# Optimization experiments

Measured on AMD Instinct MI355X. Metric: run time of the kernel, lower is better.

Reference implementation:

```python
import jax, jax.numpy as jnp
from jax import lax
import numpy as np

H, W = 28, 28
N = H * W
NMAX = 100

# gudhi CubicalComplex(top_dimensional_cells=f): lower-dim cells get the MIN of
# incident pixels (V-construction). Hence H0 of the sublevel filtration is
# connected components of pixels under 8-connectivity, where two components merge
# at the max of the connecting pixel values. H1 is computed by Alexander duality:
# dim-1 pairs of f  <->  finite dim-0 pairs of g=-f under 4-connectivity with a
# virtual outer node (g=-inf) attached to all boundary pixels; a g-pair (gb, gd)
# maps to an H1 pair (b, d) = (-gd, -gb).

def _pad_idx(Hh, Ww):
    idx = np.arange(Hh * Ww).reshape(Hh, Ww)
    p = np.full((Hh + 2, Ww + 2), -1, np.int64)
    p[1:-1, 1:-1] = idx
    return p

def _nbrs8(Hh, Ww):
    p = _pad_idx(Hh, Ww)
    dirs = [(-1, -1), (-1, 0), (-1, 1), (0, -1), (0, 1), (1, -1), (1, 0), (1, 1)]
    nb = np.full((Hh * Ww, 8), -1, np.int32)
    for k, (di, dj) in enumerate(dirs):
        nb[:, k] = p[1 + di:1 + di + Hh, 1 + dj:1 + dj + Ww].ravel()
    return nb

def _nbrs4v(Hh, Ww):
    # 4-connectivity + one slot pointing to the virtual outer node (index Hh*Ww)
    p = _pad_idx(Hh, Ww)
    dirs = [(-1, 0), (1, 0), (0, -1), (0, 1)]
    nb = np.full((Hh * Ww + 1, 5), -1, np.int32)
    for k, (di, dj) in enumerate(dirs):
        nb[:Hh * Ww, k] = p[1 + di:1 + di + Hh, 1 + dj:1 + dj + Ww].ravel()
    m = np.zeros((Hh, Ww), bool)
    m[0, :] = m[-1, :] = m[:, 0] = m[:, -1] = True
    nb[:Hh * Ww, 4] = np.where(m.ravel(), Hh * Ww, -1)
    return nb

NBRS8 = jnp.asarray(_nbrs8(H, W))
NBRS4V = jnp.asarray(_nbrs4v(H, W))

def _h0_deaths(values, nbrs):
    """Union-find over cells sorted by value; returns finite (birth, death) pairs
    (zero rows = unused slots). values: [M], nbrs: [M, K] int32 (-1 = none)."""
    M = values.shape[0]
    K = nbrs.shape[1]
    order = jnp.argsort(values)  # stable; rank = processing order (elder rule)
    rank = jnp.zeros(M, jnp.int32).at[order].set(jnp.arange(M, dtype=jnp.int32))

    def find(parent, i):
        def cond(s):
            return s[1][s[0]] != s[0]
        def body(s):
            i, p = s
            p = p.at[i].set(p[p[i]])  # path halving
            return (p[i], p)
        i, parent = lax.while_loop(cond, body, (i, parent))
        return parent, i

    def step(parent, r):
        c = order[r]
        deaths = jnp.zeros((K, 2), values.dtype)
        for k in range(K):  # fixed small unroll over neighbor slots
            n = nbrs[c, k]
            n_safe = jnp.maximum(n, 0)
            valid = (n >= 0) & (rank[n_safe] < r)  # only already-active neighbors
            parent, rc = find(parent, c)
            parent, rn = find(parent, jnp.where(valid, n_safe, c))
            merge = valid & (rc != rn)
            younger = jnp.where(rank[rc] > rank[rn], rc, rn)
            elder = jnp.where(rank[rc] > rank[rn], rn, rc)
            parent = parent.at[younger].set(jnp.where(merge, elder, younger))
            pair = jnp.stack([values[younger], values[c]])  # (birth, death)
            deaths = deaths.at[k].set(jnp.where(merge, pair, jnp.zeros(2, values.dtype)))
        return parent, deaths

    parent0 = jnp.arange(M, dtype=jnp.int32)
    _, deaths = lax.scan(step, parent0, jnp.arange(M, dtype=jnp.int32))
    return deaths.reshape(M * K, 2)

def _select_diag(pairs, nmax):
    # gudhi returns pairs sorted by decreasing persistence; min_persistence=0 drops
    # zero-persistence pairs. Pad with zeros to nmax (as the numpy diagram buffer).
    b, d = pairs[:, 0], pairs[:, 1]
    pers = jnp.where(d > b, d - b, -jnp.inf)
    v, idx = lax.top_k(pers, nmax)
    sel = pairs[idx]
    return jnp.where(v[:, None] > 0, sel, jnp.zeros_like(sel))

def _pd_sample(v0):
    # dim 0: 8-connectivity + one essential pair (global min, +inf)
    d0 = _h0_deaths(v0, NBRS8)
    ess = jnp.stack([v0.min(), jnp.array(jnp.inf, v0.dtype)])[None]
    diag0 = _select_diag(jnp.concatenate([ess, d0], axis=0), NMAX)
    # dim 1 via duality on g = -f with virtual outer node (g = -inf)
    g = jnp.concatenate([-v0, jnp.full((1,), -jnp.inf, v0.dtype)])
    dg = _h0_deaths(g, NBRS4V)
    pairs1 = jnp.stack([-dg[:, 1], -dg[:, 0]], axis=-1)  # (b, d) = (-gd, -gb)
    diag1 = _select_diag(pairs1, NMAX)
    return jnp.stack([diag0, diag1])  # [2, NMAX, 2]

def setup_inputs() -> dict:
    key = jax.random.key(0)
    x = jax.random.normal(key, (32, N), dtype=jnp.float32)
    return {"x": x}

def reference(x):
    # x: [B, H*W] -> diagrams [B, len(dimensions)=2, NMAX, 2]
    return jax.vmap(_pd_sample)(x)
```

## Files before the change

kernel.cpp:

```cpp
#include <hip/hip_runtime.h>
#include <math.h>

#define HH 28
#define WW 28
#define NPIX 784
#define MMAX 785
#define NMAXP 100
#define NTH 1024
#define BCAP 512
#define HSZ 2048
#define HMASK 2047
#define ECAP 2048
#define PCAP 512
#define JMAXP 10
#define NBUCK 4096
#define ESS_DEATH 1e30f

template<int N> struct IC { static constexpr int v = N; };

__device__ __forceinline__ unsigned f2mono(float f) {
    unsigned u = __float_as_uint(f);
    return (u & 0x80000000u) ? ~u : (u | 0x80000000u);
}
__device__ __forceinline__ float mono2f(unsigned m) {
    unsigned u = (m & 0x80000000u) ? (m ^ 0x80000000u) : ~m;
    return __uint_as_float(u);
}

__device__ __forceinline__ int get_nbrs(int c, int which, int* nb) {
    int ci = c / WW;
    int cj = c - ci * WW;
    if (which == 0) {
        const int di[8] = {-1,-1,-1, 0, 0, 1, 1, 1};
        const int dj[8] = {-1, 0, 1,-1, 1,-1, 0, 1};
        #pragma unroll
        for (int k = 0; k < 8; ++k) {
            int ii = ci + di[k], jj = cj + dj[k];
            nb[k] = (ii >= 0 && ii < HH && jj >= 0 && jj < WW) ? (ii * WW + jj) : -1;
        }
        return 8;
    } else {
        const int di[4] = {-1, 1, 0, 0};
        const int dj[4] = { 0, 0,-1, 1};
        #pragma unroll
        for (int k = 0; k < 4; ++k) {
            int ii = ci + di[k], jj = cj + dj[k];
            nb[k] = (ii >= 0 && ii < HH && jj >= 0 && jj < WW) ? (ii * WW + jj) : -1;
        }
        nb[4] = (ci == 0 || ci == HH - 1 || cj == 0 || cj == WW - 1) ? NPIX : -1;
        return 5;
    }
}

__global__ __launch_bounds__(NTH)
void pd_kernel(const float* __restrict__ x, float* __restrict__ out)
{
    const int blk   = blockIdx.x;
    const int s     = blk >> 1;
    const int which = blk & 1;
    const int tid   = threadIdx.x;
    const int lane  = tid & 63;
    const int M     = NPIX + which;

    __shared__ float vals[MMAX];
    __shared__ int   dA[MMAX];
    __shared__ int   dB[MMAX];
    __shared__ int   cido[MMAX];
    __shared__ unsigned long long rootsU[BCAP];
    __shared__ unsigned bval[BCAP];
    __shared__ unsigned hpool[2 * HSZ];
    __shared__ unsigned long long e2[ECAP];
    __shared__ unsigned long long e3[ECAP];
    __shared__ unsigned long long mrec[PCAP];
    __shared__ float pb[PCAP], pdd[PCAP];
    __shared__ int   rsel[NMAXP];
    __shared__ int   bcnt, scnt, npairs, np0g;
    __shared__ int   jflag[JMAXP + 1];
    __shared__ int   wtot[NTH / 64], wbase2[NTH / 64];

    unsigned* const hkey = hpool;
    unsigned* const hval = hpool + HSZ;
    unsigned* const cnt  = hpool;

    auto rankOf = [&](const unsigned long long* arr, int N64,
                      unsigned long long ki) -> int {
        int rk = 0;
        for (int base = 0; base < N64; base += 64) {
            unsigned long long kj = arr[base + lane];
            unsigned lo = (unsigned)kj, hi = (unsigned)(kj >> 32);
            #pragma unroll
            for (int t = 0; t < 64; ++t) {
                unsigned jlo = (unsigned)__builtin_amdgcn_readlane((int)lo, t);
                unsigned jhi = (unsigned)__builtin_amdgcn_readlane((int)hi, t);
                unsigned long long kjj = ((unsigned long long)jhi << 32) | jlo;
                rk += (kjj < ki) ? 1 : 0;
            }
        }
        return rk;
    };

    if (tid == 0) { bcnt = 0; scnt = 0; npairs = 0; np0g = 0; }
    if (tid < JMAXP + 1) jflag[tid] = 0;
    for (int i = tid; i < HSZ; i += NTH) { hkey[i] = 0u; hval[i] = 0xFFFFFFFFu; }
    for (int i = tid; i < NPIX; i += NTH) {
        float v = x[s * NPIX + i];
        vals[i] = which ? -v : v;
    }
    if (tid == 0 && which) vals[NPIX] = -INFINITY;
    __syncthreads();

    unsigned long long rku = 0ull;
    int rc = 0;
    if (tid < M) {
        int i = tid;
        int best = i; float bv = vals[i];
        if (i < NPIX) {
            int nb[8];
            int K = get_nbrs(i, which, nb);
            for (int k = 0; k < K; ++k) {
                int n = nb[k]; if (n < 0) continue;
                float vn = vals[n];
                if (vn < bv || (vn == bv && n < best)) { bv = vn; best = n; }
            }
        }
        dA[i] = best;
        if (best == i) {
            rku = ((unsigned long long)f2mono(vals[i]) << 32) | (unsigned)i;
            rc = 1;
        }
    }
    {
        int sc = rc;
        #pragma unroll
        for (int d = 1; d < 64; d <<= 1) {
            int up = __shfl_up(sc, d, 64);
            if (lane >= d) sc += up;
        }
        int wtotal = __shfl(sc, 63, 64);
        int base = 0;
        if (lane == 0 && wtotal) base = atomicAdd(&bcnt, wtotal);
        base = __shfl(base, 0, 64);
        int off = base + sc - rc;
        if (rc && off < BCAP) rootsU[off] = rku;
    }
    __syncthreads();

    int B = bcnt; if (B > BCAP) B = BCAP;
    const int B64 = (B + 63) & ~63;
    for (int i = B + tid; i < B64; i += NTH) rootsU[i] = ~0ull;

    int* rootArr = dA;
    {
        int* src = dA;
        int* dst = dB;
        for (int pass = 0; pass < JMAXP; ++pass) {
            bool changed = false;
            for (int i = tid; i < M; i += NTH) {
                int q0 = src[i];
                int q1 = src[q0];
                dst[i] = q1;
                changed |= (q1 != q0);
            }
            unsigned long long mk = __ballot(changed);
            if (lane == 0 && mk) jflag[pass] = 1;
            __syncthreads();
            rootArr = dst;
            if (!jflag[pass]) break;
            int* tmp = src; src = dst; dst = tmp;
        }
    }
    int* cidmap = (rootArr == dA) ? dB : dA;

    for (int i = tid; i < B64; i += NTH) {
        unsigned long long ki = rootsU[i];
        int rk = rankOf(rootsU, B64, ki);
        if (i < B) {
            int cell = (int)(ki & 0xFFFFFFFFull);
            cidmap[cell] = rk;
            bval[rk] = (unsigned)(ki >> 32);
        }
    }
    __syncthreads();
    for (int i = tid; i < M; i += NTH) cido[i] = cidmap[rootArr[i]];
    __syncthreads();
    int* const minF = dA;
    int* const ddp  = dA + 256;
    int* const dd2  = dB;

    for (int c = tid; c < NPIX; c += NTH) {
        float vc = vals[c];
        int bc = cido[c];
        int nb[8];
        int K = get_nbrs(c, which, nb);
        unsigned wm = f2mono(vc);
        for (int k = 0; k < K; ++k) {
            int n = nb[k]; if (n < 0) continue;
            float vn = vals[n];
            if (!(vn < vc || (vn == vc && n < c))) continue;
            int bn = cido[n];
            if (bn == bc) continue;
            unsigned c0 = (unsigned)(bc < bn ? bc : bn);
            unsigned c1 = (unsigned)(bc < bn ? bn : bc);
            unsigned pk  = (c0 << 9) | c1;
            unsigned key = pk + 1u;
            unsigned slot = (pk * 0x9E3779B1u) >> 21;
            for (;;) {
                unsigned prev = atomicCAS(&hkey[slot], 0u, key);
                if (prev == 0u || prev == key) { atomicMin(&hval[slot], wm); break; }
                slot = (slot + 1) & HMASK;
            }
        }
    }
    __syncthreads();

    {
        unsigned k0 = hkey[tid], k1 = hkey[tid + NTH];
        unsigned v0 = hval[tid], v1 = hval[tid + NTH];
        int c = (k0 ? 1 : 0) + (k1 ? 1 : 0);
        int sc = c;
        #pragma unroll
        for (int d = 1; d < 64; d <<= 1) {
            int up = __shfl_up(sc, d, 64);
            if (lane >= d) sc += up;
        }
        int wtotal = __shfl(sc, 63, 64);
        int base = 0;
        if (lane == 0 && wtotal) base = atomicAdd(&scnt, wtotal);
        base = __shfl(base, 0, 64);
        int p = base + sc - c;
        if (k0) { e2[p] = ((unsigned long long)v0 << 18) | (unsigned long long)(k0 - 1u); ++p; }
        if (k1) { e2[p] = ((unsigned long long)v1 << 18) | (unsigned long long)(k1 - 1u); ++p; }
    }
    __syncthreads();
    const int S = scnt;
    const int S64 = (S + 63) & ~63;

    for (int i = tid; i < NBUCK; i += NTH) cnt[i] = 0u;
    for (int i = S + tid; i < S64; i += NTH) { e2[i] = ~0ull; e3[i] = ~0ull; }
    __syncthreads();
    for (int i = tid; i < S; i += NTH)
        atomicAdd(&cnt[(unsigned)(e2[i] >> 38)], 1u);
    __syncthreads();
    {
        unsigned c[4]; int loc = 0;
        #pragma unroll
        for (int k2 = 0; k2 < 4; ++k2) { c[k2] = cnt[tid * 4 + k2]; loc += (int)c[k2]; }
        int scan = loc;
        #pragma unroll
        for (int d = 1; d < 64; d <<= 1) {
            int up = __shfl_up(scan, d, 64);
            if (lane >= d) scan += up;
        }
        int wid = tid >> 6;
        if (lane == 63) wtot[wid] = scan;
        __syncthreads();
        if (tid == 0) {
            int acc = 0;
            #pragma unroll
            for (int w2 = 0; w2 < NTH / 64; ++w2) { wbase2[w2] = acc; acc += wtot[w2]; }
        }
        __syncthreads();
        int ex = wbase2[wid] + (scan - loc);
        #pragma unroll
        for (int k2 = 0; k2 < 4; ++k2) { cnt[tid * 4 + k2] = (unsigned)ex; ex += (int)c[k2]; }
    }
    __syncthreads();
    for (int i = tid; i < S; i += NTH) {
        unsigned long long k = e2[i];
        unsigned slot = atomicAdd(&cnt[(unsigned)(k >> 38)], 1u);
        e3[slot] = k;
    }
    __syncthreads();
    for (int i = tid; i < S; i += NTH) {
        unsigned long long ki = e3[i];
        int b = (int)(ki >> 38);
        int lo2 = (b == 0) ? 0 : (int)cnt[b - 1];
        int hi2 = (int)cnt[b];
        int rk = lo2;
        for (int j = lo2; j < hi2; ++j) rk += (e3[j] < ki) ? 1 : 0;
        e2[rk] = ki;
    }
    if (tid < 256) { minF[tid] = 0x7FFFFFFF; ddp[tid] = tid; }
    __syncthreads();

    const bool doR1 = (B <= 256) && (S > 0);
    if (doR1) {
        for (int i = tid; i < S; i += NTH) {
            unsigned pk = (unsigned)e2[i] & 0x3FFFFu;
            atomicMin(&minF[pk >> 9], i);
            atomicMin(&minF[pk & 511u], i);
        }
    }
    __syncthreads();
    if (doR1) {
        for (int y = tid; y < B; y += NTH) {
            int fi = minF[y];
            if (fi != 0x7FFFFFFF) {
                unsigned long long k = e2[fi];
                unsigned pk = (unsigned)k & 0x3FFFFu;
                int a = (int)(pk >> 9), bq = (int)(pk & 511u);
                int z = (a == y) ? bq : a;
                if (z < y) {
                    unsigned wm = (unsigned)(k >> 18);
                    int slot = atomicAdd(&np0g, 1);
                    if (slot < PCAP)
                        mrec[slot] = ((unsigned long long)wm << 32) | (unsigned)y;
                    ddp[y] = z;
                }
            }
        }
    }
    __syncthreads();
    if (doR1) {
        for (int y = tid; y < 256; y += NTH) {
            int r = ddp[y];
            int r2 = ddp[r];
            while (r2 != r) { r = r2; r2 = ddp[r]; }
            dd2[y] = r;
        }
    }
    __syncthreads();

    auto kruskalP = [&]() {
        unsigned pl = ((unsigned)dd2[tid]) | ((unsigned)dd2[64 + tid] << 8)
                    | ((unsigned)dd2[128 + tid] << 16) | ((unsigned)dd2[192 + tid] << 24);
        int np = np0g;
        const int target = B - 1;
        for (int base = 0; base < S && np < target; base += 64) {
            unsigned long long ecache = e2[base + tid];
            unsigned eklo = (unsigned)ecache;
            unsigned ehiw = (unsigned)(ecache >> 32);
            unsigned pkL  = eklo & 0x3FFFFu;
            unsigned raaL = pkL >> 9, rbbL = pkL & 511u;
            int bpa = __builtin_amdgcn_ds_bpermute((int)((raaL & 63u) << 2), (int)pl);
            int bpb = __builtin_amdgcn_ds_bpermute((int)((rbbL & 63u) << 2), (int)pl);
            unsigned la0 = ((unsigned)bpa >> ((raaL >> 6) * 8)) & 0xFFu;
            unsigned lb0 = ((unsigned)bpb >> ((rbbL >> 6) * 8)) & 0xFFu;
            bool isc = ((base + tid) < S) && (la0 != lb0);
            unsigned long long m = __ballot(isc);
            while (m != 0ull && np < target) {
                unsigned klo[4]; int lnt[4]; unsigned la[4], lb[4]; bool act[4];
                #pragma unroll
                for (int t = 0; t < 4; ++t) {
                    act[t] = (m != 0ull);
                    int ln = act[t] ? (int)__builtin_ctzll(m) : 0;
                    if (act[t]) m &= (m - 1ull);
                    lnt[t] = ln;
                    klo[t] = (unsigned)__builtin_amdgcn_readlane((int)eklo, ln);
                    unsigned pk  = klo[t] & 0x3FFFFu;
                    unsigned raa = pk >> 9, rbb = pk & 511u;
                    unsigned kra = (unsigned)__builtin_amdgcn_readlane((int)pl, (int)(raa & 63u));
                    unsigned krb = (unsigned)__builtin_amdgcn_readlane((int)pl, (int)(rbb & 63u));
                    la[t] = (kra >> ((raa >> 6) * 8)) & 0xFFu;
                    lb[t] = (krb >> ((rbb >> 6) * 8)) & 0xFFu;
                    if (!act[t]) { la[t] = 0; lb[t] = 0; }
                }
                unsigned ys[4], es[4];
                #pragma unroll
                for (int t = 0; t < 4; ++t) {
                    unsigned A = la[t], Bv = lb[t];
                    #pragma unroll
                    for (int k = 0; k < t; ++k) {
                        A  = (A  == ys[k]) ? es[k] : A;
                        Bv = (Bv == ys[k]) ? es[k] : Bv;
                    }
                    unsigned mn = A < Bv ? A : Bv;
                    unsigned mx = A ^ Bv ^ mn;
                    es[t] = mn;
                    ys[t] = (A != Bv) ? mx : 0xFFFFFFFFu;
                }
                #pragma unroll
                for (int t = 0; t < 4; ++t) {
                    if (ys[t] != 0xFFFFFFFFu) {
                        unsigned khit = (unsigned)__builtin_amdgcn_readlane(
                            (int)ehiw, lnt[t]);
                        unsigned w = (klo[t] >> 18) | (khit << 14);
                        if (tid == 0 && np < PCAP)
                            mrec[np] = ((unsigned long long)w << 32)
                                     | (unsigned long long)ys[t];
                        ++np;
                        unsigned yr  = ys[t] * 0x01010101u;
                        unsigned xr  = (ys[t] ^ es[t]) * 0x01010101u;
                        unsigned mm  = pl ^ yr;
                        unsigned nz  = ((mm & 0x7F7F7F7Fu) + 0x7F7F7F7Fu) | mm;
                        unsigned tz  = ~nz & 0x80808080u;
                        unsigned msk = tz | (tz - (tz >> 7));
                        pl ^= (xr & msk);
                    }
                }
            }
        }
        if (tid == 0) npairs = (np < PCAP) ? np : PCAP;
    };

    auto kruskal = [&](auto icreg) {
        constexpr int NREG = decltype(icreg)::v;
        int lab[NREG];
        #pragma unroll
        for (int r = 0; r < NREG; ++r) lab[r] = r * 64 + tid;
        int np = 0;
        const int target = B - 1;
        for (int base = 0; base < S && np < target; base += 64) {
            unsigned long long ecache = e2[base + tid];
            unsigned eklo = (unsigned)ecache;
            unsigned ehiw = (unsigned)(ecache >> 32);
            unsigned pkL  = eklo & 0x3FFFFu;
            unsigned raaL = pkL >> 9, rbbL = pkL & 511u;
            int bpa[NREG], bpb[NREG];
            int aA = (int)((raaL & 63u) << 2);
            int aB = (int)((rbbL & 63u) << 2);
            #pragma unroll
            for (int r = 0; r < NREG; ++r) {
                bpa[r] = __builtin_amdgcn_ds_bpermute(aA, lab[r]);
                bpb[r] = __builtin_amdgcn_ds_bpermute(aB, lab[r]);
            }
            int la0, lb0;
            {
                unsigned sA = raaL >> 6, sB = rbbL >> 6;
                int x0 = (sA & 1) ? bpa[1] : bpa[0];
                int x1 = (sA & 1) ? bpa[3] : bpa[2];
                int x2 = (sA & 1) ? bpa[5] : bpa[4];
                int x3 = (sA & 1) ? bpa[7] : bpa[6];
                int x4 = (sA & 2) ? x1 : x0;
                int x5 = (sA & 2) ? x3 : x2;
                la0 = (sA & 4) ? x5 : x4;
                int y0 = (sB & 1) ? bpb[1] : bpb[0];
                int y1 = (sB & 1) ? bpb[3] : bpb[2];
                int y2 = (sB & 1) ? bpb[5] : bpb[4];
                int y3 = (sB & 1) ? bpb[7] : bpb[6];
                int y4 = (sB & 2) ? y1 : y0;
                int y5 = (sB & 2) ? y3 : y2;
                lb0 = (sB & 4) ? y5 : y4;
            }
            bool isc = ((base + tid) < S) && (la0 != lb0);
            unsigned long long m = __ballot(isc);
            while (m != 0ull && np < target) {
                unsigned klo[4]; int lnt[4], la[4], lb[4]; bool act[4];
                #pragma unroll
                for (int t = 0; t < 4; ++t) {
                    act[t] = (m != 0ull);
                    int ln = act[t] ? (int)__builtin_ctzll(m) : 0;
                    if (act[t]) m &= (m - 1ull);
                    lnt[t] = ln;
                    klo[t] = (unsigned)__builtin_amdgcn_readlane((int)eklo, ln);
                    unsigned pk  = klo[t] & 0x3FFFFu;
                    unsigned raa = pk >> 9, rbb = pk & 511u;
                    int sa = (int)(raa >> 6), sb = (int)(rbb >> 6);
                    asm volatile("" : "+v"(sa), "+v"(sb));
                    int a1 = (sa & 1) ? lab[1] : lab[0];
                    int b1 = (sa & 1) ? lab[3] : lab[2];
                    int c1 = (sa & 1) ? lab[5] : lab[4];
                    int d1 = (sa & 1) ? lab[7] : lab[6];
                    int e1 = (sa & 2) ? b1 : a1;
                    int f1 = (sa & 2) ? d1 : c1;
                    int g1 = (sa & 4) ? f1 : e1;
                    int a2 = (sb & 1) ? lab[1] : lab[0];
                    int b2 = (sb & 1) ? lab[3] : lab[2];
                    int c2 = (sb & 1) ? lab[5] : lab[4];
                    int d2 = (sb & 1) ? lab[7] : lab[6];
                    int e2v = (sb & 2) ? b2 : a2;
                    int f2 = (sb & 2) ? d2 : c2;
                    int g2 = (sb & 4) ? f2 : e2v;
                    la[t] = __builtin_amdgcn_readlane(g1, (int)(raa & 63u));
                    lb[t] = __builtin_amdgcn_readlane(g2, (int)(rbb & 63u));
                    if (!act[t]) { la[t] = 0; lb[t] = 0; }
                }
                int ys[4], es[4];
                #pragma unroll
                for (int t = 0; t < 4; ++t) {
                    int A = la[t], Bv = lb[t];
                    #pragma unroll
                    for (int k = 0; k < t; ++k) {
                        A  = (A  == ys[k]) ? es[k] : A;
                        Bv = (Bv == ys[k]) ? es[k] : Bv;
                    }
                    int mn = A < Bv ? A : Bv;
                    int mx = A ^ Bv ^ mn;
                    es[t] = mn;
                    ys[t] = (A != Bv) ? mx : -1;
                }
                #pragma unroll
                for (int t = 0; t < 4; ++t) {
                    if (ys[t] >= 0) {
                        unsigned khit = (unsigned)__builtin_amdgcn_readlane(
                            (int)ehiw, lnt[t]);
                        unsigned w = (klo[t] >> 18) | (khit << 14);
                        if (tid == 0 && np < PCAP)
                            mrec[np] = ((unsigned long long)w << 32) | (unsigned)ys[t];
                        ++np;
                        #pragma unroll
                        for (int r = 0; r < NREG; ++r)
                            lab[r] = (lab[r] == ys[t]) ? es[t] : lab[r];
                    }
                }
            }
        }
        if (tid == 0) npairs = (np < PCAP) ? np : PCAP;
    };

    if (tid < 64 && S > 0) {
        if (B <= 256) kruskalP();
        else          kruskal(IC<8>{});
    }
    __syncthreads();
    const int P = npairs;
    const int P64 = (P + 63) & ~63;

    for (int i = tid; i < P64; i += NTH) {
        unsigned long long kk2 = ~0ull;
        if (i < P) {
            unsigned long long m = mrec[i];
            int y = (int)(m & 0xFFFFFFFFull);
            float w  = mono2f((unsigned)(m >> 32));
            float bf = mono2f(bval[y]);
            float b, d;
            if (which == 0) { b = bf; d = w; }
            else            { b = -w; d = -bf; }
            pb[i] = b; pdd[i] = d;
            unsigned pm = __float_as_uint(d - b);
            kk2 = ((unsigned long long)(~pm) << 32) | (unsigned)i;
        }
        e2[i] = kk2;
    }
    if (tid < NMAXP) rsel[tid] = -1;
    __syncthreads();

    const int off = (which == 0) ? 1 : 0;
    for (int i = tid; i < P64; i += NTH) {
        unsigned long long ki = e2[i];
        int rk = rankOf(e2, P64, ki);
        if (i < P && rk < NMAXP - off) rsel[rk + off] = i;
    }
    __syncthreads();

    float* o = out + (size_t)blk * NMAXP * 2;
    if (tid < NMAXP) {
        float b = 0.f, d = 0.f;
        if (which == 0 && tid == 0) { b = mono2f(bval[0]); d = ESS_DEATH; }
        else {
            int q = rsel[tid];
            if (q >= 0) { b = pb[q]; d = pdd[q]; }
        }
        o[tid * 2]     = b;
        o[tid * 2 + 1] = d;
    }
}

extern "C" void kernel_launch(void* const* d_in, const int* in_sizes, int n_in,
                              void* d_out, int out_size, void* d_ws, size_t ws_size,
                              hipStream_t stream) {
    (void)in_sizes; (void)n_in; (void)out_size; (void)d_ws; (void)ws_size;
    const float* x = (const float*)d_in[0];
    float* out = (float*)d_out;
    pd_kernel<<<dim3(64), dim3(NTH), 0, stream>>>(x, out);
}
```

Before: 80.04 us.

## Fuse pointer jumping with root ranking and cut barriers in edge bucket sort

Pointer jumping now runs in place on one array, with several hops per iteration. Root ranking is folded into the first iteration, which removes the ping-pong buffers and a separate pass. The bucket histogram is built while edges are compacted, using half as many buckets from a dedicated shared array. The serial warp-base scan is replaced by a per-thread prefix over warp totals, and the minF atomics are merged into the ranking loop. All of this removes several __syncthreads and passes, at the cost of in-place races in the jumping (benign for convergence) and larger buckets for the rank scan.

```diff
diff --git a/kernel.cpp b/kernel.cpp
--- a/kernel.cpp
+++ b/kernel.cpp
@@ -12,8 +12,8 @@
 #define HMASK 2047
 #define ECAP 2048
 #define PCAP 512
-#define JMAXP 10
-#define NBUCK 4096
+#define JITER 6
+#define NBUCK 2048
 #define ESS_DEATH 1e30f
 
 template<int N> struct IC { static constexpr int v = N; };
@@ -69,24 +69,25 @@
     __shared__ unsigned long long rootsU[BCAP];
     __shared__ unsigned bval[BCAP];
     __shared__ unsigned hpool[2 * HSZ];
+    __shared__ unsigned cnt[NBUCK];
     __shared__ unsigned long long e2[ECAP];
     __shared__ unsigned long long e3[ECAP];
     __shared__ unsigned long long mrec[PCAP];
     __shared__ float pb[PCAP], pdd[PCAP];
     __shared__ int   rsel[NMAXP];
     __shared__ int   bcnt, scnt, npairs, np0g;
-    __shared__ int   jflag[JMAXP + 1];
-    __shared__ int   wtot[NTH / 64], wbase2[NTH / 64];
+    __shared__ int   jflag[JITER];
+    __shared__ int   wtot[NTH / 64];
 
     unsigned* const hkey = hpool;
     unsigned* const hval = hpool + HSZ;
-    unsigned* const cnt  = hpool;
-
-    auto rankOf = [&](const unsigned long long* arr, int N64,
+
+    auto rankOf = [&](const unsigned long long* arr, int N,
                       unsigned long long ki) -> int {
         int rk = 0;
+        int N64 = (N + 63) & ~63;
         for (int base = 0; base < N64; base += 64) {
-            unsigned long long kj = arr[base + lane];
+            unsigned long long kj = (base + lane < N) ? arr[base + lane] : ~0ull;
             unsigned lo = (unsigned)kj, hi = (unsigned)(kj >> 32);
             #pragma unroll
             for (int t = 0; t < 64; ++t) {
@@ -100,8 +101,9 @@
     };
 
     if (tid == 0) { bcnt = 0; scnt = 0; npairs = 0; np0g = 0; }
-    if (tid < JMAXP + 1) jflag[tid] = 0;
+    if (tid < JITER) jflag[tid] = 0;
     for (int i = tid; i < HSZ; i += NTH) { hkey[i] = 0u; hval[i] = 0xFFFFFFFFu; }
+    for (int i = tid; i < NBUCK; i += NTH) cnt[i] = 0u;
     for (int i = tid; i < NPIX; i += NTH) {
         float v = x[s * NPIX + i];
         vals[i] = which ? -v : v;
@@ -147,41 +149,38 @@
 
     int B = bcnt; if (B > BCAP) B = BCAP;
     const int B64 = (B + 63) & ~63;
-    for (int i = B + tid; i < B64; i += NTH) rootsU[i] = ~0ull;
-
-    int* rootArr = dA;
-    {
-        int* src = dA;
-        int* dst = dB;
-        for (int pass = 0; pass < JMAXP; ++pass) {
-            bool changed = false;
-            for (int i = tid; i < M; i += NTH) {
-                int q0 = src[i];
-                int q1 = src[q0];
-                dst[i] = q1;
-                changed |= (q1 != q0);
-            }
-            unsigned long long mk = __ballot(changed);
-            if (lane == 0 && mk) jflag[pass] = 1;
-            __syncthreads();
-            rootArr = dst;
-            if (!jflag[pass]) break;
-            int* tmp = src; src = dst; dst = tmp;
-        }
-    }
-    int* cidmap = (rootArr == dA) ? dB : dA;
-
-    for (int i = tid; i < B64; i += NTH) {
-        unsigned long long ki = rootsU[i];
-        int rk = rankOf(rootsU, B64, ki);
-        if (i < B) {
-            int cell = (int)(ki & 0xFFFFFFFFull);
-            cidmap[cell] = rk;
-            bval[rk] = (unsigned)(ki >> 32);
-        }
-    }
-    __syncthreads();
-    for (int i = tid; i < M; i += NTH) cido[i] = cidmap[rootArr[i]];
+
+    for (int it = 0; it < JITER; ++it) {
+        if (tid < M) {
+            #pragma unroll
+            for (int r = 0; r < 3; ++r) {
+                int q = dA[tid]; int r2 = dA[q];
+                if (r2 != q) dA[tid] = r2;
+            }
+        }
+        if (it == 0) {
+            for (int i = tid; i < B64; i += NTH) {
+                unsigned long long ki = rootsU[i];
+                int rk = rankOf(rootsU, B, ki);
+                if (i < B) {
+                    dB[(int)(ki & 0xFFFFFFFFull)] = rk;
+                    bval[rk] = (unsigned)(ki >> 32);
+                }
+            }
+        }
+        __syncthreads();
+        bool changed = false;
+        if (tid < M) {
+            int q = dA[tid]; int r2 = dA[q];
+            if (r2 != q) { dA[tid] = r2; changed = true; }
+        }
+        unsigned long long mk = __ballot(changed);
+        if (lane == 0 && mk) jflag[it] = 1;
+        __syncthreads();
+        if (!jflag[it]) break;
+    }
+
+    for (int i = tid; i < M; i += NTH) cido[i] = dB[dA[i]];
     __syncthreads();
     int* const minF = dA;
     int* const ddp  = dA + 256;
@@ -228,23 +227,26 @@
         if (lane == 0 && wtotal) base = atomicAdd(&scnt, wtotal);
         base = __shfl(base, 0, 64);
         int p = base + sc - c;
-        if (k0) { e2[p] = ((unsigned long long)v0 << 18) | (unsigned long long)(k0 - 1u); ++p; }
-        if (k1) { e2[p] = ((unsigned long long)v1 << 18) | (unsigned long long)(k1 - 1u); ++p; }
+        if (k0) {
+            e2[p] = ((unsigned long long)v0 << 18) | (unsigned long long)(k0 - 1u);
+            atomicAdd(&cnt[v0 >> 21], 1u); ++p;
+        }
+        if (k1) {
+            e2[p] = ((unsigned long long)v1 << 18) | (unsigned long long)(k1 - 1u);
+            atomicAdd(&cnt[v1 >> 21], 1u); ++p;
+        }
     }
     __syncthreads();
     const int S = scnt;
     const int S64 = (S + 63) & ~63;
-
-    for (int i = tid; i < NBUCK; i += NTH) cnt[i] = 0u;
-    for (int i = S + tid; i < S64; i += NTH) { e2[i] = ~0ull; e3[i] = ~0ull; }
-    __syncthreads();
-    for (int i = tid; i < S; i += NTH)
-        atomicAdd(&cnt[(unsigned)(e2[i] >> 38)], 1u);
-    __syncthreads();
+    const bool doR1 = (B <= 256) && (S > 0);
+
     {
-        unsigned c[4]; int loc = 0;
-        #pragma unroll
-        for (int k2 = 0; k2 < 4; ++k2) { c[k2] = cnt[tid * 4 + k2]; loc += (int)c[k2]; }
+        for (int i = S + tid; i < S64; i += NTH) e2[i] = ~0ull;
+        if (tid < 256) { minF[tid] = 0x7FFFFFFF; ddp[tid] = tid; }
+        unsigned c[2]; int loc = 0;
+        #pragma unroll
+        for (int k2 = 0; k2 < 2; ++k2) { c[k2] = cnt[tid * 2 + k2]; loc += (int)c[k2]; }
         int scan = loc;
         #pragma unroll
         for (int d = 1; d < 64; d <<= 1) {
@@ -254,44 +256,35 @@
         int wid = tid >> 6;
         if (lane == 63) wtot[wid] = scan;
         __syncthreads();
-        if (tid == 0) {
-            int acc = 0;
-            #pragma unroll
-            for (int w2 = 0; w2 < NTH / 64; ++w2) { wbase2[w2] = acc; acc += wtot[w2]; }
-        }
-        __syncthreads();
-        int ex = wbase2[wid] + (scan - loc);
-        #pragma unroll
-        for (int k2 = 0; k2 < 4; ++k2) { cnt[tid * 4 + k2] = (unsigned)ex; ex += (int)c[k2]; }
+        int wb = 0;
+        for (int w2 = 0; w2 < wid; ++w2) wb += wtot[w2];
+        int ex = wb + (scan - loc);
+        #pragma unroll
+        for (int k2 = 0; k2 < 2; ++k2) { cnt[tid * 2 + k2] = (unsigned)ex; ex += (int)c[k2]; }
     }
     __syncthreads();
     for (int i = tid; i < S; i += NTH) {
         unsigned long long k = e2[i];
-        unsigned slot = atomicAdd(&cnt[(unsigned)(k >> 38)], 1u);
+        unsigned slot = atomicAdd(&cnt[(unsigned)(k >> 39)], 1u);
         e3[slot] = k;
     }
     __syncthreads();
     for (int i = tid; i < S; i += NTH) {
         unsigned long long ki = e3[i];
-        int b = (int)(ki >> 38);
+        int b = (int)(ki >> 39);
         int lo2 = (b == 0) ? 0 : (int)cnt[b - 1];
         int hi2 = (int)cnt[b];
         int rk = lo2;
         for (int j = lo2; j < hi2; ++j) rk += (e3[j] < ki) ? 1 : 0;
         e2[rk] = ki;
-    }
-    if (tid < 256) { minF[tid] = 0x7FFFFFFF; ddp[tid] = tid; }
-    __syncthreads();
-
-    const bool doR1 = (B <= 256) && (S > 0);
-    if (doR1) {
-        for (int i = tid; i < S; i += NTH) {
-            unsigned pk = (unsigned)e2[i] & 0x3FFFFu;
-            atomicMin(&minF[pk >> 9], i);
-            atomicMin(&minF[pk & 511u], i);
-        }
-    }
-    __syncthreads();
+        if (doR1) {
+            unsigned pk = (unsigned)ki & 0x3FFFFu;
+            atomicMin(&minF[pk >> 9], rk);
+            atomicMin(&minF[pk & 511u], rk);
+        }
+    }
+    __syncthreads();
+
     if (doR1) {
         for (int y = tid; y < B; y += NTH) {
             int fi = minF[y];
```

After: 85.89 us. 1.07x slower.
